# Optimization experiments

Hardware: AMD Instinct MI355X
Metric: run time of the kernel (lower is better)

Reference implementation:

```python
import jax, jax.numpy as jnp
import numpy as np

B, D, C = 8192, 1024, 4096  # batch, d_model, num_clusters (all active)
EPS = 1e-12  # matches F.normalize eps


def _l2_normalize(x):
    n = jnp.linalg.norm(x, axis=-1, keepdims=True)
    return x / jnp.maximum(n, EPS)


def setup_inputs() -> dict:
    key = jax.random.key(0)
    k1, k2 = jax.random.split(key)
    embedding = jax.random.normal(k1, (B, D), dtype=jnp.float32)
    centroids = jax.random.normal(k2, (C, D), dtype=jnp.float32)  # buffer, all active
    return {"embedding": embedding, "centroids": centroids}


def reference(embedding, centroids):
    # Fused equivalent of the per-centroid Python loop:
    # cosine sim of normalized embedding vs each normalized centroid.
    emb_n = _l2_normalize(embedding)        # [B, D]
    cen_n = _l2_normalize(centroids)        # [C, D]
    sims = jnp.clip(emb_n @ cen_n.T, 0.0, 1.0)  # [B, C], per-sim clamp to [0,1]
    max_sim = jnp.max(sims, axis=-1)        # [B]
    closest = jnp.argmax(sims, axis=-1)     # [B] int
    novelty = jnp.clip(jnp.sqrt(1.0 - max_sim), 0.0, 1.0)  # [B]
    return novelty, closest
```

## Files before the change

kernel.cpp:

```cpp
#include <hip/hip_runtime.h>
#include <math.h>

#define B_ROWS 8192
#define C_COLS 4096
#define D_DIM  1024
#define EPSN   1e-12f

typedef float v4f __attribute__((ext_vector_type(4)));
typedef short v8s __attribute__((ext_vector_type(8)));

__device__ __forceinline__ unsigned short bf16_rtn(float x) {
    unsigned int u = __float_as_uint(x);
    u += 0x7fffu + ((u >> 16) & 1u);
    return (unsigned short)(u >> 16);
}

__device__ __forceinline__ bool better_vi(float v, int i, float V, int I) {
    return (v > V) || (v == V && i < I);
}

__global__ __launch_bounds__(256) void prep_kernel(
    const float* __restrict__ emb, const float* __restrict__ cen,
    unsigned short* __restrict__ Ah, unsigned short* __restrict__ Bh,
    float* __restrict__ inv_a, float* __restrict__ inv_b)
{
    const int lane = threadIdx.x & 63;
    const int wid  = blockIdx.x * 4 + (threadIdx.x >> 6);
    const float* src; unsigned short* dst; float* invp; int r;
    if (wid < B_ROWS) { src = emb; r = wid;          dst = Ah; invp = inv_a; }
    else              { src = cen; r = wid - B_ROWS; dst = Bh; invp = inv_b; }

    const float* rp = src + (size_t)r * D_DIM;
    float4 v[4];
    float ss = 0.0f;
    #pragma unroll
    for (int j = 0; j < 4; ++j) {
        v[j] = *(const float4*)(rp + (j * 64 + lane) * 4);
        ss += v[j].x * v[j].x + v[j].y * v[j].y + v[j].z * v[j].z + v[j].w * v[j].w;
    }
    #pragma unroll
    for (int off = 1; off < 64; off <<= 1) ss += __shfl_xor(ss, off, 64);

    const float iv = 1.0f / fmaxf(sqrtf(ss), EPSN);
    if (lane == 0) invp[r] = iv;

    unsigned short* dp = dst + (size_t)r * D_DIM;
    #pragma unroll
    for (int j = 0; j < 4; ++j) {
        ushort4 H;
        H.x = bf16_rtn(v[j].x * iv);
        H.y = bf16_rtn(v[j].y * iv);
        H.z = bf16_rtn(v[j].z * iv);
        H.w = bf16_rtn(v[j].w * iv);
        *(ushort4*)(dp + (j * 64 + lane) * 4) = H;
    }
}

#define GLD16(gp, lp) \
    __builtin_amdgcn_global_load_lds( \
        (const __attribute__((address_space(1))) void*)(gp), \
        (__attribute__((address_space(3))) void*)(lp), 16, 0, 0)

__global__ __launch_bounds__(512, 2) void simmax_kernel(
    const unsigned short* __restrict__ Ahg, const unsigned short* __restrict__ Bhg,
    float* __restrict__ p1v, int* __restrict__ p1i,
    float* __restrict__ p2v, int* __restrict__ p2i)
{
    __shared__ unsigned short lds[2 * 32768];

    const int tid    = threadIdx.x;
    const int L      = tid & 63;
    const int w      = tid >> 6;
    const int lane15 = L & 15;
    const int quad   = L >> 4;
    const int wr     = w >> 2;
    const int wc     = w & 3;

    const int bid = blockIdx.x;
    const int c   = bid & 7, s = bid >> 3;
    const int gx  = ((c & 3) << 3) + (s & 7);
    const int gy  = ((c >> 2) << 3) + (s >> 3);
    const int row0 = gx * 256;
    const int c0   = gy * 256;

    const int scol = (tid & 7) ^ ((tid >> 3) & 7);
    const unsigned short* aB = Ahg + (size_t)(row0 + (tid >> 3)) * D_DIM + scol * 8;
    const unsigned short* bB = Bhg + (size_t)(c0   + (tid >> 3)) * D_DIM + scol * 8;
    const int wofs = w * 512;

#define STAGE_ALL(bo, kb) do { \
    GLD16(aB + (kb),           &lds[(bo) + 0     + wofs]); \
    GLD16(aB + 65536  + (kb),  &lds[(bo) + 4096  + wofs]); \
    GLD16(aB + 131072 + (kb),  &lds[(bo) + 8192  + wofs]); \
    GLD16(aB + 196608 + (kb),  &lds[(bo) + 12288 + wofs]); \
    GLD16(bB + (kb),           &lds[(bo) + 16384 + wofs]); \
    GLD16(bB + 65536  + (kb),  &lds[(bo) + 20480 + wofs]); \
    GLD16(bB + 131072 + (kb),  &lds[(bo) + 24576 + wofs]); \
    GLD16(bB + 196608 + (kb),  &lds[(bo) + 28672 + wofs]); \
} while (0)

    v4f acc[8][4];
    #pragma unroll
    for (int mt = 0; mt < 8; ++mt)
        #pragma unroll
        for (int nt = 0; nt < 4; ++nt) acc[mt][nt] = (v4f)0.0f;

    int rA[8], rB[4];
    #pragma unroll
    for (int t = 0; t < 8; ++t) rA[t] = (wr * 128 + t * 16 + lane15) * 64;
    #pragma unroll
    for (int t = 0; t < 4; ++t) rB[t] = 16384 + (wc * 64 + t * 16 + lane15) * 64;
    const int s7  = lane15 & 7;
    const int cq0 = (quad ^ s7) * 8;
    const int cq1 = ((4 + quad) ^ s7) * 8;

    STAGE_ALL(0, 0);
    __syncthreads();

    int cur = 0;
    for (int t = 0; t < 16; ++t) {
        const int bo = cur << 15;
        if (t < 15) STAGE_ALL(32768 - bo, (t + 1) * 64);

        #pragma unroll
        for (int h = 0; h < 2; ++h) {
            const int cq = h ? cq1 : cq0;
            v8s fb[4], fa[8];
            #pragma unroll
            for (int nt = 0; nt < 4; ++nt) fb[nt] = *(const v8s*)&lds[bo + rB[nt] + cq];
            #pragma unroll
            for (int mt = 0; mt < 8; ++mt) fa[mt] = *(const v8s*)&lds[bo + rA[mt] + cq];
            #pragma unroll
            for (int mt = 0; mt < 8; ++mt)
                #pragma unroll
                for (int nt = 0; nt < 4; ++nt)
                    acc[mt][nt] = __builtin_amdgcn_mfma_f32_16x16x32_bf16(
                        fa[mt], fb[nt], acc[mt][nt], 0, 0, 0);
        }
        if (t < 15) __syncthreads();
        cur ^= 1;
    }

    const int pc = gy * 4 + wc;
    #pragma unroll
    for (int mt = 0; mt < 8; ++mt) {
        #pragma unroll
        for (int r = 0; r < 4; ++r) {
            float a1v = acc[mt][0][r];
            int   a1i = c0 + wc * 64 + 0 * 16 + lane15;
            float a2v = -1e30f;
            int   a2i = 0x7fffffff;
            #pragma unroll
            for (int nt = 1; nt < 4; ++nt) {
                float v  = acc[mt][nt][r];
                int   ci = c0 + wc * 64 + nt * 16 + lane15;
                if (better_vi(v, ci, a1v, a1i))      { a2v = a1v; a2i = a1i; a1v = v; a1i = ci; }
                else if (better_vi(v, ci, a2v, a2i)) { a2v = v;   a2i = ci; }
            }
            #pragma unroll
            for (int off = 8; off; off >>= 1) {
                float b1v = __shfl_down(a1v, off, 64); int b1i = __shfl_down(a1i, off, 64);
                float b2v = __shfl_down(a2v, off, 64); int b2i = __shfl_down(a2i, off, 64);
                if (better_vi(b1v, b1i, a1v, a1i)) {
                    if (better_vi(a1v, a1i, b2v, b2i)) { a2v = a1v; a2i = a1i; }
                    else                               { a2v = b2v; a2i = b2i; }
                    a1v = b1v; a1i = b1i;
                } else if (better_vi(b1v, b1i, a2v, a2i)) {
                    a2v = b1v; a2i = b1i;
                }
            }
            if (lane15 == 0) {
                int rg = row0 + wr * 128 + mt * 16 + quad * 4 + r;
                size_t ix = (size_t)rg * 64 + pc;
                p1v[ix] = a1v; p1i[ix] = a1i;
                p2v[ix] = a2v; p2i[ix] = a2i;
            }
        }
    }
}

__global__ __launch_bounds__(256) void finalize_kernel(
    const float* __restrict__ emb, const float* __restrict__ cen,
    const float* __restrict__ inv_a, const float* __restrict__ inv_b,
    const float* __restrict__ p1v, const int* __restrict__ p1i,
    const float* __restrict__ p2v, const int* __restrict__ p2i,
    float* __restrict__ out)
{
    const int lane = threadIdx.x & 63;
    const int row  = blockIdx.x * 4 + (threadIdx.x >> 6);
    const size_t base = (size_t)row * 64 + lane;

    float v[4]; int ix[4];
    v[0] = p1v[base]; ix[0] = p1i[base];
    v[1] = p2v[base]; ix[1] = p2i[base];
    v[2] = -1e30f;    ix[2] = 0x7ffffffe;
    v[3] = -1e30f;    ix[3] = 0x7fffffff;

    #pragma unroll
    for (int off = 1; off < 64; off <<= 1) {
        float ov[4]; int oi[4];
        #pragma unroll
        for (int k = 0; k < 4; ++k) {
            ov[k] = __shfl_xor(v[k],  off, 64);
            oi[k] = __shfl_xor(ix[k], off, 64);
        }
        #pragma unroll
        for (int k = 0; k < 4; ++k) {
            float bv = ov[k]; int bi = oi[k];
            bool b0 = better_vi(bv, bi, v[0], ix[0]);
            bool b1 = better_vi(bv, bi, v[1], ix[1]);
            bool b2 = better_vi(bv, bi, v[2], ix[2]);
            bool b3 = better_vi(bv, bi, v[3], ix[3]);
            float nv3 = b2 ? v[2] : (b3 ? bv : v[3]); int ni3 = b2 ? ix[2] : (b3 ? bi : ix[3]);
            float nv2 = b1 ? v[1] : (b2 ? bv : v[2]); int ni2 = b1 ? ix[1] : (b2 ? bi : ix[2]);
            float nv1 = b0 ? v[0] : (b1 ? bv : v[1]); int ni1 = b0 ? ix[0] : (b1 ? bi : ix[1]);
            float nv0 = b0 ? bv   : v[0];             int ni0 = b0 ? bi    : ix[0];
            v[0] = nv0; ix[0] = ni0; v[1] = nv1; ix[1] = ni1;
            v[2] = nv2; ix[2] = ni2; v[3] = nv3; ix[3] = ni3;
        }
    }

    const float* er = emb + (size_t)row * D_DIM;
    const float* cr0 = cen + (size_t)ix[0] * D_DIM;
    const float* cr1 = cen + (size_t)ix[1] * D_DIM;
    const float* cr2 = cen + (size_t)ix[2] * D_DIM;
    const float* cr3 = cen + (size_t)ix[3] * D_DIM;

    float d[4] = { 0.0f, 0.0f, 0.0f, 0.0f };
    #pragma unroll
    for (int j = 0; j < 4; ++j) {
        int e = (j * 64 + lane) * 4;
        float4 ev = *(const float4*)(er  + e);
        float4 c0 = *(const float4*)(cr0 + e);
        float4 c1 = *(const float4*)(cr1 + e);
        float4 c2 = *(const float4*)(cr2 + e);
        float4 c3 = *(const float4*)(cr3 + e);
        d[0] += ev.x * c0.x + ev.y * c0.y + ev.z * c0.z + ev.w * c0.w;
        d[1] += ev.x * c1.x + ev.y * c1.y + ev.z * c1.z + ev.w * c1.w;
        d[2] += ev.x * c2.x + ev.y * c2.y + ev.z * c2.z + ev.w * c2.w;
        d[3] += ev.x * c3.x + ev.y * c3.y + ev.z * c3.z + ev.w * c3.w;
    }
    #pragma unroll
    for (int off = 1; off < 64; off <<= 1) {
        #pragma unroll
        for (int c = 0; c < 4; ++c) d[c] += __shfl_xor(d[c], off, 64);
    }

    if (lane == 0) {
        const float ia = inv_a[row];
        float m = -1e30f; int ci = 0x7fffffff;
        #pragma unroll
        for (int c = 0; c < 4; ++c) {
            float s = d[c] * ia * inv_b[ix[c]];
            if (better_vi(s, ix[c], m, ci)) { m = s; ci = ix[c]; }
        }
        if (m <= 0.0f) ci = 0;
        float ms = fminf(fmaxf(m, 0.0f), 1.0f);
        out[row]          = fminf(fmaxf(sqrtf(1.0f - ms), 0.0f), 1.0f);
        out[B_ROWS + row] = (float)ci;
    }
}

extern "C" void kernel_launch(void* const* d_in, const int* in_sizes, int n_in,
                              void* d_out, int out_size, void* d_ws, size_t ws_size,
                              hipStream_t stream)
{
    const float* emb = (const float*)d_in[0];
    const float* cen = (const float*)d_in[1];
    float* out = (float*)d_out;

    unsigned short* Ahp = (unsigned short*)d_ws;
    unsigned short* Bhp = Ahp + (size_t)B_ROWS * D_DIM;
    float* inv_a = (float*)(Bhp + (size_t)C_COLS * D_DIM);
    float* inv_b = inv_a + B_ROWS;
    float* p1v   = inv_b + C_COLS;
    int*   p1i   = (int*)(p1v + (size_t)64 * B_ROWS);
    float* p2v   = (float*)(p1i + (size_t)64 * B_ROWS);
    int*   p2i   = (int*)(p2v + (size_t)64 * B_ROWS);

    prep_kernel<<<(B_ROWS + C_COLS) / 4, 256, 0, stream>>>(emb, cen, Ahp, Bhp, inv_a, inv_b);

    simmax_kernel<<<dim3(512), 512, 0, stream>>>(Ahp, Bhp, p1v, p1i, p2v, p2i);

    finalize_kernel<<<B_ROWS / 4, 256, 0, stream>>>(emb, cen, inv_a, inv_b,
                                                    p1v, p1i, p2v, p2i, out);
}
```

Measured before the change: 222.5 us.

## Split GEMM main loop into four barrier-gated phases interleaving prefetch with MFMA

Restructures the double-buffered K loop into four sub-phases. Each phase loads a quarter of the fragments from LDS, issues two of the next tile's global-to-LDS loads, then runs 16 MFMAs at raised wave priority. Explicit vmcnt/lgkmcnt waits, s_barrier and sched_barrier replace the single __syncthreads and bulk staging, so global loads spread across the compute. This aims to overlap memory traffic with matrix math and cut the number of fragment registers live at once. The price is more barriers per iteration and hand-tuned wait counts that must match the load order exactly.

```diff
diff --git a/kernel.cpp b/kernel.cpp
--- a/kernel.cpp
+++ b/kernel.cpp
@@ -88,16 +88,14 @@
     const unsigned short* bB = Bhg + (size_t)(c0   + (tid >> 3)) * D_DIM + scol * 8;
     const int wofs = w * 512;
 
-#define STAGE_ALL(bo, kb) do { \
-    GLD16(aB + (kb),           &lds[(bo) + 0     + wofs]); \
-    GLD16(aB + 65536  + (kb),  &lds[(bo) + 4096  + wofs]); \
-    GLD16(aB + 131072 + (kb),  &lds[(bo) + 8192  + wofs]); \
-    GLD16(aB + 196608 + (kb),  &lds[(bo) + 12288 + wofs]); \
-    GLD16(bB + (kb),           &lds[(bo) + 16384 + wofs]); \
-    GLD16(bB + 65536  + (kb),  &lds[(bo) + 20480 + wofs]); \
-    GLD16(bB + 131072 + (kb),  &lds[(bo) + 24576 + wofs]); \
-    GLD16(bB + 196608 + (kb),  &lds[(bo) + 28672 + wofs]); \
-} while (0)
+#define STG_A0(bo, kb) GLD16(aB + (kb),           &lds[(bo) + 0     + wofs])
+#define STG_A1(bo, kb) GLD16(aB + 65536  + (kb),  &lds[(bo) + 4096  + wofs])
+#define STG_A2(bo, kb) GLD16(aB + 131072 + (kb),  &lds[(bo) + 8192  + wofs])
+#define STG_A3(bo, kb) GLD16(aB + 196608 + (kb),  &lds[(bo) + 12288 + wofs])
+#define STG_B0(bo, kb) GLD16(bB + (kb),           &lds[(bo) + 16384 + wofs])
+#define STG_B1(bo, kb) GLD16(bB + 65536  + (kb),  &lds[(bo) + 20480 + wofs])
+#define STG_B2(bo, kb) GLD16(bB + 131072 + (kb),  &lds[(bo) + 24576 + wofs])
+#define STG_B3(bo, kb) GLD16(bB + 196608 + (kb),  &lds[(bo) + 28672 + wofs])
 
     v4f acc[8][4];
     #pragma unroll
@@ -114,31 +112,82 @@
     const int cq0 = (quad ^ s7) * 8;
     const int cq1 = ((4 + quad) ^ s7) * 8;
 
-    STAGE_ALL(0, 0);
-    __syncthreads();
-
-    int cur = 0;
+    STG_A0(0, 0); STG_A2(0, 0);
+    STG_B0(0, 0); STG_B1(0, 0); STG_B2(0, 0); STG_B3(0, 0);
+    STG_A1(0, 0); STG_A3(0, 0);
+
     for (int t = 0; t < 16; ++t) {
-        const int bo = cur << 15;
-        if (t < 15) STAGE_ALL(32768 - bo, (t + 1) * 64);
-
-        #pragma unroll
-        for (int h = 0; h < 2; ++h) {
-            const int cq = h ? cq1 : cq0;
-            v8s fb[4], fa[8];
-            #pragma unroll
-            for (int nt = 0; nt < 4; ++nt) fb[nt] = *(const v8s*)&lds[bo + rB[nt] + cq];
-            #pragma unroll
-            for (int mt = 0; mt < 8; ++mt) fa[mt] = *(const v8s*)&lds[bo + rA[mt] + cq];
-            #pragma unroll
-            for (int mt = 0; mt < 8; ++mt)
-                #pragma unroll
-                for (int nt = 0; nt < 4; ++nt)
-                    acc[mt][nt] = __builtin_amdgcn_mfma_f32_16x16x32_bf16(
-                        fa[mt], fb[nt], acc[mt][nt], 0, 0, 0);
-        }
-        if (t < 15) __syncthreads();
-        cur ^= 1;
+        const int  bo_c = (t & 1) << 15;
+        const int  bo_n = bo_c ^ 32768;
+        const int  kb1  = (t + 1) * 64;
+        const bool pf   = (t < 15);
+
+        v8s fa[4], fb0[4], fb1[4];
+
+        asm volatile("s_waitcnt vmcnt(2)" ::: "memory");
+        __builtin_amdgcn_s_barrier();
+        __builtin_amdgcn_sched_barrier(0);
+        #pragma unroll
+        for (int n = 0; n < 4; ++n) fb0[n] = *(const v8s*)&lds[bo_c + rB[n] + cq0];
+        #pragma unroll
+        for (int m = 0; m < 4; ++m) fa[m]  = *(const v8s*)&lds[bo_c + rA[m] + cq0];
+        if (pf) { STG_A0(bo_n, kb1); STG_A2(bo_n, kb1); }
+        asm volatile("s_waitcnt lgkmcnt(0)" ::: "memory");
+        __builtin_amdgcn_sched_barrier(0);
+        __builtin_amdgcn_s_setprio(1);
+        #pragma unroll
+        for (int m = 0; m < 4; ++m)
+            #pragma unroll
+            for (int n = 0; n < 4; ++n)
+                acc[m][n] = __builtin_amdgcn_mfma_f32_16x16x32_bf16(fa[m], fb0[n], acc[m][n], 0, 0, 0);
+        __builtin_amdgcn_s_setprio(0);
+
+        __builtin_amdgcn_s_barrier();
+        #pragma unroll
+        for (int n = 0; n < 4; ++n) fb1[n] = *(const v8s*)&lds[bo_c + rB[n] + cq1];
+        #pragma unroll
+        for (int m = 0; m < 4; ++m) fa[m]  = *(const v8s*)&lds[bo_c + rA[m] + cq1];
+        if (pf) { STG_B0(bo_n, kb1); STG_B1(bo_n, kb1); }
+        asm volatile("s_waitcnt lgkmcnt(0)" ::: "memory");
+        __builtin_amdgcn_sched_barrier(0);
+        __builtin_amdgcn_s_setprio(1);
+        #pragma unroll
+        for (int m = 0; m < 4; ++m)
+            #pragma unroll
+            for (int n = 0; n < 4; ++n)
+                acc[m][n] = __builtin_amdgcn_mfma_f32_16x16x32_bf16(fa[m], fb1[n], acc[m][n], 0, 0, 0);
+        __builtin_amdgcn_s_setprio(0);
+
+        if (pf) asm volatile("s_waitcnt vmcnt(4)" ::: "memory");
+        else    asm volatile("s_waitcnt vmcnt(0)" ::: "memory");
+        __builtin_amdgcn_s_barrier();
+        __builtin_amdgcn_sched_barrier(0);
+        #pragma unroll
+        for (int m = 0; m < 4; ++m) fa[m] = *(const v8s*)&lds[bo_c + rA[4 + m] + cq0];
+        if (pf) { STG_B2(bo_n, kb1); STG_B3(bo_n, kb1); }
+        asm volatile("s_waitcnt lgkmcnt(0)" ::: "memory");
+        __builtin_amdgcn_sched_barrier(0);
+        __builtin_amdgcn_s_setprio(1);
+        #pragma unroll
+        for (int m = 0; m < 4; ++m)
+            #pragma unroll
+            for (int n = 0; n < 4; ++n)
+                acc[4 + m][n] = __builtin_amdgcn_mfma_f32_16x16x32_bf16(fa[m], fb0[n], acc[4 + m][n], 0, 0, 0);
+        __builtin_amdgcn_s_setprio(0);
+
+        __builtin_amdgcn_s_barrier();
+        #pragma unroll
+        for (int m = 0; m < 4; ++m) fa[m] = *(const v8s*)&lds[bo_c + rA[4 + m] + cq1];
+        if (pf) { STG_A1(bo_n, kb1); STG_A3(bo_n, kb1); }
+        asm volatile("s_waitcnt lgkmcnt(0)" ::: "memory");
+        __builtin_amdgcn_sched_barrier(0);
+        __builtin_amdgcn_s_setprio(1);
+        #pragma unroll
+        for (int m = 0; m < 4; ++m)
+            #pragma unroll
+            for (int n = 0; n < 4; ++n)
+                acc[4 + m][n] = __builtin_amdgcn_mfma_f32_16x16x32_bf16(fa[m], fb1[n], acc[4 + m][n], 0, 0, 0);
+        __builtin_amdgcn_s_setprio(0);
     }
 
     const int pc = gy * 4 + wc;
```

Result: no change. 219.7 us (-1.3%).
